# Kernel optimization log

Hardware: AMD Instinct MI355X
Metric: run time of the kernel (lower is better)

Reference implementation:

```python
import jax, jax.numpy as jnp
import numpy as np

B, N, M = 8, 1024, 64          # graphs, ops/graph, machines/graph
OPF, MF = 16, 8                # raw feature dims
H, D, L = 8, 64, 3             # heads, head dim, HGT layers
F = H * D                      # 512 = hidden_dim * num_heads
KC = 8                         # compatible machines per op
NOP, NM = B * N, B * M
EPS = 1e-5


def _graph_ln(x, w, b):
    # PyG LayerNorm(mode='graph') with batch=None: scalar mean/std over the whole tensor
    x = x - x.mean()
    return x / (x.std() + EPS) * w + b


def _seg_softmax(a, idx, n):
    amax = jax.ops.segment_max(a, idx, num_segments=n)
    amax = jnp.where(jnp.isfinite(amax), amax, 0.0)
    ex = jnp.exp(a - amax[idx])
    s = jax.ops.segment_sum(ex, idx, num_segments=n)
    return ex / (s[idx] + 1e-16)


def _forward(op_x, machine_x, W_emb_op, b_emb_op, W_emb_m, b_emb_m,
             opn_w, opn_b, mn_w, mn_b, Wk, bk, Wq, bq, Wv, bv,
             A_rel, M_rel, p_rel, W_out, b_out, skip, ln_w, ln_b,
             ei_precedes, ei_canproc, ei_compat):
    x_op = _graph_ln(op_x @ W_emb_op + b_emb_op, opn_w, opn_b)
    x_m = _graph_ln(machine_x @ W_emb_m + b_emb_m, mn_w, mn_b)
    s0, d0 = ei_precedes   # op -> op
    s1, d1 = ei_canproc    # machine -> op
    s2, d2 = ei_compat     # op -> machine
    scale = 1.0 / jnp.sqrt(jnp.float32(D))
    for l in range(L):
        k_op = (x_op @ Wk[l, 0] + bk[l, 0]).reshape(NOP, H, D)
        q_op = (x_op @ Wq[l, 0] + bq[l, 0]).reshape(NOP, H, D)
        v_op = (x_op @ Wv[l, 0] + bv[l, 0]).reshape(NOP, H, D)
        k_m = (x_m @ Wk[l, 1] + bk[l, 1]).reshape(NM, H, D)
        q_m = (x_m @ Wq[l, 1] + bq[l, 1]).reshape(NM, H, D)
        v_m = (x_m @ Wv[l, 1] + bv[l, 1]).reshape(NM, H, D)
        # relation-specific per-head transforms (a_rel/m_rel of HGTConv)
        k0 = jnp.einsum('nhd,hde->nhe', k_op, A_rel[l, 0]); v0 = jnp.einsum('nhd,hde->nhe', v_op, M_rel[l, 0])
        k1 = jnp.einsum('nhd,hde->nhe', k_m, A_rel[l, 1]);  v1 = jnp.einsum('nhd,hde->nhe', v_m, M_rel[l, 1])
        k2 = jnp.einsum('nhd,hde->nhe', k_op, A_rel[l, 2]); v2 = jnp.einsum('nhd,hde->nhe', v_op, M_rel[l, 2])
        # attention into op nodes: joint softmax over both incoming edge types
        a0 = (q_op[d0] * k0[s0]).sum(-1) * p_rel[l, 0] * scale   # [E0,H]
        a1 = (q_op[d1] * k1[s1]).sum(-1) * p_rel[l, 1] * scale   # [E1,H]
        a_op = jnp.concatenate([a0, a1]); dd = jnp.concatenate([d0, d1])
        w = _seg_softmax(a_op, dd, NOP)
        msg = jnp.concatenate([v0[s0], v1[s1]]) * w[:, :, None]
        agg_op = jax.ops.segment_sum(msg, dd, num_segments=NOP).reshape(NOP, F)
        # attention into machine nodes
        a2 = (q_m[d2] * k2[s2]).sum(-1) * p_rel[l, 2] * scale
        w2 = _seg_softmax(a2, d2, NM)
        agg_m = jax.ops.segment_sum(v2[s2] * w2[:, :, None], d2, num_segments=NM).reshape(NM, F)
        # output projection + learned skip gate (HGTConv internals)
        o_op = jax.nn.gelu(agg_op, approximate=False) @ W_out[l, 0] + b_out[l, 0]
        o_m = jax.nn.gelu(agg_m, approximate=False) @ W_out[l, 1] + b_out[l, 1]
        g_op = jax.nn.sigmoid(skip[l, 0]); g_m = jax.nn.sigmoid(skip[l, 1])
        o_op = g_op * o_op + (1.0 - g_op) * x_op
        o_m = g_m * o_m + (1.0 - g_m) * x_m
        # wrapper residual + dropout(eval=identity) + graph layer norm
        x_op = _graph_ln(o_op + x_op, ln_w[l], ln_b[l])
        x_m = _graph_ln(o_m + x_m, ln_w[l], ln_b[l])
    fea_j = x_op.reshape(B, N, F)
    fea_m = x_m.reshape(B, M, F)
    return fea_j, fea_m, fea_j.mean(1, keepdims=True), fea_m.mean(1, keepdims=True)


def setup_inputs() -> dict:
    key = jax.random.key(0)
    ks = jax.random.split(key, 12)
    rng = np.random.default_rng(0)
    ids = np.arange(NOP).reshape(B, N)
    src0 = ids[:, :-1].ravel(); dst0 = ids[:, 1:].ravel()
    mach = rng.integers(0, M, size=(B, N, KC)) + (np.arange(B) * M)[:, None, None]
    ops = np.broadcast_to(ids[:, :, None], (B, N, KC))
    ei_precedes = jnp.asarray(np.stack([src0, dst0]), dtype=jnp.int32)
    ei_canproc = jnp.asarray(np.stack([mach.ravel(), ops.ravel()]), dtype=jnp.int32)
    ei_compat = jnp.asarray(np.stack([ops.ravel(), mach.ravel()]), dtype=jnp.int32)
    n = lambda k, sh, s=0.05: jax.random.normal(k, sh, dtype=jnp.float32) * s
    return dict(
        op_x=n(ks[0], (NOP, OPF), 1.0),
        machine_x=n(ks[1], (NM, MF), 1.0),
        W_emb_op=n(ks[2], (OPF, F)), b_emb_op=jnp.zeros((F,), jnp.float32),
        W_emb_m=n(ks[3], (MF, F)), b_emb_m=jnp.zeros((F,), jnp.float32),
        opn_w=jnp.ones((F,), jnp.float32), opn_b=jnp.zeros((F,), jnp.float32),
        mn_w=jnp.ones((F,), jnp.float32), mn_b=jnp.zeros((F,), jnp.float32),
        Wk=n(ks[4], (L, 2, F, F)), bk=jnp.zeros((L, 2, F), jnp.float32),
        Wq=n(ks[5], (L, 2, F, F)), bq=jnp.zeros((L, 2, F), jnp.float32),
        Wv=n(ks[6], (L, 2, F, F)), bv=jnp.zeros((L, 2, F), jnp.float32),
        A_rel=n(ks[7], (L, 3, H, D, D)), M_rel=n(ks[8], (L, 3, H, D, D)),
        p_rel=jnp.ones((L, 3, H), jnp.float32),
        W_out=n(ks[9], (L, 2, F, F)), b_out=jnp.zeros((L, 2, F), jnp.float32),
        skip=jnp.ones((L, 2), jnp.float32),
        ln_w=jnp.ones((L, F), jnp.float32), ln_b=jnp.zeros((L, F), jnp.float32),
        ei_precedes=ei_precedes, ei_canproc=ei_canproc, ei_compat=ei_compat,
    )


def reference(op_x, machine_x, W_emb_op, b_emb_op, W_emb_m, b_emb_m,
              opn_w, opn_b, mn_w, mn_b, Wk, bk, Wq, bq, Wv, bv,
              A_rel, M_rel, p_rel, W_out, b_out, skip, ln_w, ln_b,
              ei_precedes, ei_canproc, ei_compat):
    return _forward(op_x, machine_x, W_emb_op, b_emb_op, W_emb_m, b_emb_m,
                    opn_w, opn_b, mn_w, mn_b, Wk, bk, Wq, bq, Wv, bv,
                    A_rel, M_rel, p_rel, W_out, b_out, skip, ln_w, ln_b,
                    ei_precedes, ei_canproc, ei_compat)
```

## Files before the change

### kernel.cpp

```cpp
#include <hip/hip_runtime.h>

typedef unsigned short u16;
typedef __attribute__((ext_vector_type(4))) float floatx4;
typedef __attribute__((ext_vector_type(8))) short shortx8;
typedef __attribute__((ext_vector_type(4))) short shortx4;

#define NOPS 8192
#define NMS  512
#define CQ   2560
#define CM   1536
#define NE2  65536
#define TOPC (NOPS*512)
#define TMC  (NMS*512)

__device__ __forceinline__ float bf2f(u16 u){ return __uint_as_float(((unsigned)u)<<16); }
__device__ __forceinline__ u16 f2bf(float f){
  unsigned u = __float_as_uint(f);
  u += 0x7FFFu + ((u>>16)&1u);
  return (u16)(u>>16);
}
__device__ __forceinline__ float wred(float v){
  #pragma unroll
  for (int o=32;o;o>>=1) v += __shfl_xor(v,o,64);
  return v;
}
__device__ __forceinline__ float wredmax(float v){
  #pragma unroll
  for (int o=32;o;o>>=1) v = fmaxf(v, __shfl_xor(v,o,64));
  return v;
}
__device__ __forceinline__ float geluf(float x){
  return 0.5f*x*(1.f+erff(x*0.70710678118654752f));
}
__device__ __forceinline__ void block_stat_out2(float s, float s2, float* pstat, int slot){
  __shared__ float sb[8];
  s = wred(s); s2 = wred(s2);
  int wv = threadIdx.x >> 6;
  if ((threadIdx.x & 63) == 0){ sb[wv*2] = s; sb[wv*2+1] = s2; }
  __syncthreads();
  if (threadIdx.x == 0){
    float a = 0.f, b = 0.f;
    int nw = blockDim.x >> 6;
    for (int i=0;i<nw;++i){ a += sb[i*2]; b += sb[i*2+1]; }
    pstat[slot*2]   = a;
    pstat[slot*2+1] = b;
  }
}

__global__ __launch_bounds__(256) void cnt2_k(const int* __restrict__ s1, float* __restrict__ Ct,
                                              float* __restrict__ Cn){
  int idx = blockIdx.x*256 + threadIdx.x;
  int n = idx >> 6, l = idx & 63;
  const int* row = s1 + n*8;
  int cnt = 0;
  #pragma unroll
  for (int j=0;j<8;++j) cnt += ((row[j] & 63) == l);
  float f = (float)cnt;
  Cn[(size_t)n*64 + l] = f;
  int b = n >> 10, nl = n & 1023;
  Ct[(size_t)((b<<6) + l)*1024 + nl] = f;
}

__global__ __launch_bounds__(256) void tw_k(const float* __restrict__ Wout, const float* __restrict__ Wq,
                                            u16* __restrict__ Wout_t, u16* __restrict__ Wc_op_t,
                                            u16* __restrict__ Wc_m_t){
  __shared__ u16 t[64][65];
  int g = blockIdx.x;
  const float* s; u16* d;
  if (g < 6){
    s = Wout + (size_t)g*262144;
    d = Wout_t + (size_t)g*262144;
  } else {
    int blk = g - 6; int l = blk >> 1, side = blk & 1;
    s = Wq + (size_t)blk*262144;
    d = side ? (Wc_m_t + (size_t)l*CM*512) : (Wc_op_t + (size_t)l*CQ*512);
  }
  int kb = blockIdx.y*64, nb = blockIdx.z*64;
  int tx = threadIdx.x & 63, ty4 = threadIdx.x >> 6;
  #pragma unroll 4
  for (int p=0;p<16;++p){
    int k = ty4 + p*4;
// ... 78 lines not shown
      int ccl = wn*64 + nt*16 + mrow;
      #pragma unroll
      for (int r2=0;r2<4;++r2){
        int e = wm*32 + mt*16 + quad*4 + r2;
        Wt[(size_t)(rbase + e)*512 + cc0 + ccl] = f2bf(acc[mt][nt][r2]);
      }
    }
  }
}
__global__ void cbias_k(const float* __restrict__ bk, const float* __restrict__ bv,
                        const float* __restrict__ Ar, const float* __restrict__ Mr,
                        float* bias_op, float* bias_m){
  int gx = blockIdx.x; int e = threadIdx.x;
  int l = gx/48; int rem = gx - l*48; int s = rem >> 3; int h = rem & 7;
  int side = (s < 4) ? 0 : 1;
  int r = (s < 4) ? (s+1) : (s-3);
  int useK = side==0 ? (s==0 || s==2) : (s==4);
  int rel  = side==0 ? ((s<2)?0:2) : 1;
  const float* bb  = (useK ? bk : bv) + (size_t)(l*2+side)*512 + h*64;
  const float* Rel = (useK ? Ar : Mr) + ((size_t)(l*3+rel)*8 + h)*4096;
  float acc = 0.f;
  for (int d=0; d<64; ++d) acc += bb[d]*Rel[d*64 + e];
  float* bias = side ? (bias_m + l*CM) : (bias_op + l*CQ);
  bias[r*512 + h*64 + e] = acc;
}

__global__ __launch_bounds__(256) void embed2_k(const float* __restrict__ Xop, const float* __restrict__ Wop,
                                                const float* __restrict__ bop, float* __restrict__ Yop,
                                                const float* __restrict__ Xm, const float* __restrict__ Wm,
                                                const float* __restrict__ bm_, float* __restrict__ Ym,
                                                float* pstat, float* pstat_m){
  int bid = blockIdx.x;
  const float *X, *W, *bias; float *Y, *ps; int K, total, nb, lb;
  if (bid < 1024){ X=Xop; W=Wop; bias=bop; Y=Yop; ps=pstat;   K=16; total=TOPC; nb=1024; lb=bid; }
  else           { X=Xm;  W=Wm;  bias=bm_; Y=Ym;  ps=pstat_m; K=8;  total=TMC;  nb=128;  lb=bid-1024; }
  float s = 0.f, s2 = 0.f;
  for (int idx = lb*256 + threadIdx.x; idx < total; idx += nb*256){
    int n = idx >> 9, f = idx & 511;
    float v = bias[f];
    for (int c=0;c<K;++c) v += X[n*K+c] * W[c*512+f];
    Y[idx] = v;
    s += v; s2 += v*v;
  }
  block_stat_out2(s, s2, ps, lb);
}

__global__ __launch_bounds__(256) void ln2_k(const float* __restrict__ src_op, float* __restrict__ dst_op,
                                             u16* __restrict__ dbf_op, const float* __restrict__ w_op,
                                             const float* __restrict__ b_op,
                                             const float* __restrict__ src_m, float* __restrict__ dst_m,
                                             u16* __restrict__ dbf_m, const float* __restrict__ w_m,
                                             const float* __restrict__ b_m,
                                             const float* __restrict__ pstat, const float* __restrict__ pstat_m,
                                             int nbo, int nbm){
  int bid = blockIdx.x;
  const float *src, *w, *b, *ps; float* dst; u16* dbf; int total4, nb, lb, nblk; float inv_n;
  if (bid < 1024){ src=src_op; dst=dst_op; dbf=dbf_op; w=w_op; b=b_op; ps=pstat;
                   total4=TOPC/4; nb=1024; lb=bid; nblk=nbo; inv_n=1.f/TOPC; }
  else           { src=src_m;  dst=dst_m;  dbf=dbf_m;  w=w_m;  b=b_m;  ps=pstat_m;
                   total4=TMC/4;  nb=128;  lb=bid-1024; nblk=nbm; inv_n=1.f/TMC; }
  __shared__ float sb[8];
  __shared__ float mr[2];
  float s = 0.f, s2 = 0.f;
  for (int i = threadIdx.x; i < nblk; i += 256){ s += ps[2*i]; s2 += ps[2*i+1]; }
  s = wred(s); s2 = wred(s2);
  int wv = threadIdx.x >> 6;
  if ((threadIdx.x & 63) == 0){ sb[wv*2] = s; sb[wv*2+1] = s2; }
  __syncthreads();
  if (threadIdx.x == 0){
    float a = 0.f, bsum = 0.f;
    for (int i=0;i<4;++i){ a += sb[i*2]; bsum += sb[i*2+1]; }
    float mean = a * inv_n;
    float var  = fmaxf(bsum * inv_n - mean*mean, 0.f);
    mr[0] = mean;
    mr[1] = 1.f/(sqrtf(var) + 1e-5f);
  }
  __syncthreads();
  float mean = mr[0], rinv = mr[1];
  const floatx4* s4 = (const floatx4*)src;
  floatx4* d4 = (floatx4*)dst;
  shortx4* db4 = (shortx4*)dbf;
  const floatx4* w4 = (const floatx4*)w;
  const floatx4* b4 = (const floatx4*)b;
  for (int i = lb*256 + threadIdx.x; i < total4; i += nb*256){
    int f = i & 127;
    floatx4 v = s4[i], wv2 = w4[f], bv = b4[f];
    shortx4 sv;
    #pragma unroll
    for (int e=0;e<4;++e){ v[e] = (v[e]-mean)*rinv*wv2[e] + bv[e]; sv[e] = (short)f2bf(v[e]); }
    d4[i] = v;
    db4[i] = sv;
  }
}

__device__ __forceinline__ void gemm_gate_core(u16* As, u16* Bs, const u16* __restrict__ A,
                                               const u16* __restrict__ Bt,
                                               const float* __restrict__ xr, const float* __restrict__ bo,
                                               const float* __restrict__ sk, float* __restrict__ Y,
                                               float* pstat, int slot, int bx, int by){
  const int tid = threadIdx.x;
  const int lane = tid & 63, wave = tid >> 6;
  const int bm = by * 128, bn = bx * 128;
  const int wm = wave & 1, wn = wave >> 1;
  const int mrow = lane & 15, quad = lane >> 4;
  const u16* Ab = A + (size_t)bm*512;
  const u16* Bb = Bt + (size_t)bn*512;
  floatx4 acc[4][4];
  #pragma unroll
  for (int a=0;a<4;++a)
    #pragma unroll
    for (int b=0;b<4;++b) acc[a][b] = (floatx4){0.f,0.f,0.f,0.f};
  const int r0 = tid >> 2, c0 = (tid & 3) * 8;
  const int r1 = (tid+256) >> 2, c1 = ((tid+256) & 3) * 8;
  const int lds0 = wave*512;
  const int lds1 = wave*512 + 2048;
  for (int k0 = 0; k0 < 512; k0 += 32){
    __builtin_amdgcn_global_load_lds((const __attribute__((address_space(1))) void*)(Ab + (size_t)r0*512 + k0 + c0),
                                     (__attribute__((address_space(3))) void*)(As + lds0), 16, 0, 0);
    __builtin_amdgcn_global_load_lds((const __attribute__((address_space(1))) void*)(Ab + (size_t)r1*512 + k0 + c1),
                                     (__attribute__((address_space(3))) void*)(As + lds1), 16, 0, 0);
    __builtin_amdgcn_global_load_lds((const __attribute__((address_space(1))) void*)(Bb + (size_t)r0*512 + k0 + c0),
                                     (__attribute__((address_space(3))) void*)(Bs + lds0), 16, 0, 0);
    __builtin_amdgcn_global_load_lds((const __attribute__((address_space(1))) void*)(Bb + (size_t)r1*512 + k0 + c1),
                                     (__attribute__((address_space(3))) void*)(Bs + lds1), 16, 0, 0);
    __syncthreads();
    shortx8 af[4], bf[4];
    #pragma unroll
    for (int mt=0;mt<4;++mt) af[mt] = *(const shortx8*)(As + (wm*64 + mt*16 + mrow)*32 + quad*8);
    #pragma unroll
    for (int nt=0;nt<4;++nt) bf[nt] = *(const shortx8*)(Bs + (wn*64 + nt*16 + mrow)*32 + quad*8);
    #pragma unroll
    for (int mt=0;mt<4;++mt)
      #pragma unroll
      for (int nt=0;nt<4;++nt)
        acc[mt][nt] = __builtin_amdgcn_mfma_f32_16x16x32_bf16(af[mt], bf[nt], acc[mt][nt], 0, 0, 0);
    __syncthreads();
  }
  float g = 1.f/(1.f+expf(-(*sk)));
  float s = 0.f, s2 = 0.f;
  #pragma unroll
  for (int mt=0;mt<4;++mt){
    #pragma unroll
    for (int nt=0;nt<4;++nt){
      int col = bn + wn*64 + nt*16 + mrow;
// ... 100 lines not shown
    for (int mt=0;mt<4;++mt) af[mt] = *(const shortx8*)(a0 + mt*512);
    #pragma unroll
    for (int nt=0;nt<4;++nt) bf[nt] = *(const shortx8*)(b0 + nt*512);
    stage_half8(Ab, kc1, Obase + 8192, tid);
    MFMA_QUAD(0);
    __builtin_amdgcn_s_barrier();

    #pragma unroll
    for (int mt=0;mt<4;++mt) af[mt] = *(const shortx8*)(a0 + 2048 + mt*512);
    stage_half8(Bb, kc1, Obase + 24576, tid);
    MFMA_QUAD(1);
    asm volatile("s_waitcnt vmcnt(8)" ::: "memory");
    __builtin_amdgcn_s_barrier();

    #pragma unroll
    for (int mt=0;mt<4;++mt) af[mt] = *(const shortx8*)(a0 + 8192 + mt*512);
    #pragma unroll
    for (int nt=0;nt<4;++nt) bf[nt] = *(const shortx8*)(b0 + 8192 + nt*512);
    stage_half8(Ab, kc2, Sbase, tid);
    MFMA_QUAD(0);
    __builtin_amdgcn_s_barrier();

    #pragma unroll
    for (int mt=0;mt<4;++mt) af[mt] = *(const shortx8*)(a0 + 8192 + 2048 + mt*512);
    stage_half8(Bb, kc2, Sbase + 16384, tid);
    MFMA_QUAD(1);
    asm volatile("s_waitcnt vmcnt(8)" ::: "memory");
    __builtin_amdgcn_s_barrier();
  }

  const int crow0 = by*256 + wm*128 + quad*4;
  const int ccol0 = bx*256 + wn*64 + mrow;
  float bv[4];
  #pragma unroll
  for (int nt=0;nt<4;++nt) bv[nt] = bias ? bias[ccol0 + nt*16] : 0.f;
  #pragma unroll
  for (int mh=0;mh<2;++mh){
    #pragma unroll
    for (int mt=0;mt<4;++mt){
      int row = crow0 + mh*64 + mt*16;
      #pragma unroll
      for (int nt=0;nt<4;++nt){
        int col = ccol0 + nt*16;
        #pragma unroll
        for (int r2=0;r2<4;++r2)
          C[(size_t)(row+r2)*N + col] = f2bf(acc[mh*4+mt][nt][r2] + bv[nt]);
      }
    }
  }
}

__global__ __launch_bounds__(256) void qk12_k(const u16* __restrict__ qkv_op, const u16* __restrict__ qkv_m,
                                              const float* __restrict__ prel, const float* __restrict__ Cn,
                                              float* __restrict__ S2f, u16* __restrict__ agg_op){
  __shared__ __align__(16) char smem[37376];
  u16* smem16 = (u16*)smem;
  u16* As = smem16;
  u16* Bs = smem16 + 4608;
  float* Sbuf = (float*)smem;
  u16* P   = smem16 + 9216;
  u16* v1T = smem16 + 13824;
  float* wpreS = (float*)(smem + 36864);
  float* linvS = (float*)(smem + 37120);
  int bh = blockIdx.y; int b = bh >> 3, h = bh & 7;
  int n0 = blockIdx.x * 64;
  int tid = threadIdx.x, lane = tid & 63, wave = tid >> 6;
  int mrow = lane & 15, quad = lane >> 4;
  int wm = wave & 1, wn = wave >> 1;
  int srow = tid >> 2, scol = (tid & 3) * 16;
  if (blockIdx.z == 0){
    float p1 = prel[8 + h] * 0.125f;
    {
      const u16* src = qkv_op + (size_t)(b*1024 + n0 + srow)*CQ + h*64 + scol;
      *(shortx8*)(As + srow*72 + scol)     = *(const shortx8*)(src);
      *(shortx8*)(As + srow*72 + scol + 8) = *(const shortx8*)(src + 8);
    }
    {
      const u16* src = qkv_m + (size_t)(b*64 + srow)*CM + 512 + h*64 + scol;
      *(shortx8*)(Bs + srow*72 + scol)     = *(const shortx8*)(src);
      *(shortx8*)(Bs + srow*72 + scol + 8) = *(const shortx8*)(src + 8);
    }
    {
      const u16* src = qkv_m + (size_t)(b*64 + srow)*CM + 1024 + h*64 + scol;
      shortx8 v0 = *(const shortx8*)(src);
      shortx8 v1 = *(const shortx8*)(src + 8);
      #pragma unroll
      for (int e=0;e<8;++e){ v1T[(scol+e)*72 + srow] = (u16)v0[e]; v1T[(scol+8+e)*72 + srow] = (u16)v1[e]; }
    }
    __syncthreads();
    floatx4 acc[2][2];
    #pragma unroll
    for (int a=0;a<2;++a){ acc[a][0] = (floatx4){0,0,0,0}; acc[a][1] = (floatx4){0,0,0,0}; }
    #pragma unroll
    for (int ks=0; ks<2; ++ks){
      shortx8 af[2], bf[2];
      #pragma unroll
      for (int mt=0;mt<2;++mt) af[mt] = *(const shortx8*)(As + (wm*32 + mt*16 + mrow)*72 + ks*32 + quad*8);
      #pragma unroll
      for (int nt=0;nt<2;++nt) bf[nt] = *(const shortx8*)(Bs + (wn*32 + nt*16 + mrow)*72 + ks*32 + quad*8);
      #pragma unroll
      for (int mt=0;mt<2;++mt)
        #pragma unroll
        for (int nt=0;nt<2;++nt)
          acc[mt][nt] = __builtin_amdgcn_mfma_f32_16x16x32_bf16(af[mt], bf[nt], acc[mt][nt], 0, 0, 0);
    }
    __syncthreads();
    #pragma unroll
    for (int mt=0;mt<2;++mt){
      #pragma unroll
      for (int nt=0;nt<2;++nt){
        int m = wn*32 + nt*16 + mrow;
        #pragma unroll
        for (int r2=0;r2<4;++r2){
          int nl = wm*32 + mt*16 + quad*4 + r2;
          Sbuf[nl*66 + m] = acc[mt][nt][r2] * p1;
        }
      }
    }
    __syncthreads();
    {
      int row = srow;
      int mb  = scol;
      int n_g = b*1024 + n0 + row;
      int nl  = n0 + row;
      float sp = -1e30f;
      if (nl > 0){
        float p0 = prel[h] * 0.125f;
        const u16* qp = qkv_op + (size_t)n_g*CQ + h*64 + mb;
        const u16* kp = qkv_op + (size_t)(n_g-1)*CQ + 512 + h*64 + mb;
        shortx8 qa = *(const shortx8*)(qp), qb2 = *(const shortx8*)(qp + 8);
        shortx8 ka = *(const shortx8*)(kp), kb2 = *(const shortx8*)(kp + 8);
        float d = 0.f;
        #pragma unroll
        for (int e=0;e<8;++e) d += bf2f((u16)qa[e])*bf2f((u16)ka[e]) + bf2f((u16)qb2[e])*bf2f((u16)kb2[e]);
        d += __shfl_xor(d, 1, 64);
        d += __shfl_xor(d, 2, 64);
        sp = d * p0;
      }
      const float* crow = Cn + (size_t)n_g*64 + mb;
      float cv[16];
      float mx = sp;
      #pragma unroll
      for (int j=0;j<16;++j){
        cv[j] = crow[j];
        if (cv[j] > 0.f) mx = fmaxf(mx, Sbuf[row*66 + mb + j]);
      }
      mx = fmaxf(mx, __shfl_xor(mx, 1, 64));
      mx = fmaxf(mx, __shfl_xor(mx, 2, 64));
      float L = 0.f;
      #pragma unroll
      for (int j=0;j<16;j+=4){
        shortx4 pv;
        #pragma unroll
        for (int e=0;e<4;++e){
          float w = (cv[j+e] > 0.f) ? cv[j+e]*expf(Sbuf[row*66 + mb + j + e] - mx) : 0.f;
          L += w;
          pv[e] = (short)f2bf(w);
        }
        *(shortx4*)(P + row*72 + mb + j) = pv;
      }
      L += __shfl_xor(L, 1, 64);
      L += __shfl_xor(L, 2, 64);
      float ep = (nl > 0) ? expf(sp - mx) : 0.f;
      L += ep;
      if ((tid & 3) == 0){ wpreS[row] = ep; linvS[row] = 1.f/(L + 1e-16f); }
    }
    __syncthreads();
    floatx4 po[2][2];
    #pragma unroll
    for (int a=0;a<2;++a){ po[a][0] = (floatx4){0,0,0,0}; po[a][1] = (floatx4){0,0,0,0}; }
    #pragma unroll
    for (int ks=0; ks<2; ++ks){
      shortx8 paf[2], pbf[2];
      #pragma unroll
      for (int mt=0;mt<2;++mt) paf[mt] = *(const shortx8*)(P + (wm*32 + mt*16 + mrow)*72 + ks*32 + quad*8);
      #pragma unroll
      for (int nt=0;nt<2;++nt) pbf[nt] = *(const shortx8*)(v1T + (wn*32 + nt*16 + mrow)*72 + ks*32 + quad*8);
      #pragma unroll
      for (int mt=0;mt<2;++mt)
        #pragma unroll
        for (int nt=0;nt<2;++nt)
          po[mt][nt] = __builtin_amdgcn_mfma_f32_16x16x32_bf16(paf[mt], pbf[nt], po[mt][nt], 0, 0, 0);
    }
    #pragma unroll
    for (int mt=0;mt<2;++mt){
      #pragma unroll
      for (int nt=0;nt<2;++nt){
        int d = wn*32 + nt*16 + mrow;
        #pragma unroll
        for (int r2=0;r2<4;++r2){
          int rl = wm*32 + mt*16 + quad*4 + r2;
          int n = n0 + rl;
          size_t ng = (size_t)b*1024 + n;
          float v = po[mt][nt][r2];
          if (n > 0) v += wpreS[rl] * bf2f(qkv_op[(ng-1)*CQ + 1024 + h*64 + d]);
          v *= linvS[rl];
          agg_op[ng*512 + h*64 + d] = f2bf(geluf(v));
        }
      }
    }
  } else {
    float p2 = prel[16 + h] * 0.125f;
    {
      const u16* src = qkv_m + (size_t)(b*64 + srow)*CM + h*64 + scol;
      *(shortx8*)(As + srow*72 + scol)     = *(const shortx8*)(src);
      *(shortx8*)(As + srow*72 + scol + 8) = *(const shortx8*)(src + 8);
    }
    {
      const u16* src = qkv_op + (size_t)(b*1024 + n0 + srow)*CQ + 1536 + h*64 + scol;
      *(shortx8*)(Bs + srow*72 + scol)     = *(const shortx8*)(src);
      *(shortx8*)(Bs + srow*72 + scol + 8) = *(const shortx8*)(src + 8);
    }
    __syncthreads();
    floatx4 acc[2][2];
    #pragma unroll
    for (int a=0;a<2;++a){ acc[a][0] = (floatx4){0,0,0,0}; acc[a][1] = (floatx4){0,0,0,0}; }
    #pragma unroll
    for (int ks=0; ks<2; ++ks){
      shortx8 af[2], bf[2];
      #pragma unroll
      for (int mt=0;mt<2;++mt) af[mt] = *(const shortx8*)(As + (wm*32 + mt*16 + mrow)*72 + ks*32 + quad*8);
      #pragma unroll
      for (int nt=0;nt<2;++nt) bf[nt] = *(const shortx8*)(Bs + (wn*32 + nt*16 + mrow)*72 + ks*32 + quad*8);
      #pragma unroll
      for (int mt=0;mt<2;++mt)
        #pragma unroll
        for (int nt=0;nt<2;++nt)
          acc[mt][nt] = __builtin_amdgcn_mfma_f32_16x16x32_bf16(af[mt], bf[nt], acc[mt][nt], 0, 0, 0);
    }
    #pragma unroll
    for (int mt=0;mt<2;++mt){
      #pragma unroll
      for (int nt=0;nt<2;++nt){
        int n = wn*32 + nt*16 + mrow;
        #pragma unroll
        for (int r2=0;r2<4;++r2){
          int m = wm*32 + mt*16 + quad*4 + r2;
          S2f[((size_t)(b*64 + m)*8 + h)*1024 + n0 + n] = acc[mt][nt][r2] * p2;
        }
      }
    }
  }
}

__global__ __launch_bounds__(512) void msoftm_k(const float* __restrict__ S2f, const float* __restrict__ Ct,
                                                u16* __restrict__ W2){
  int m = blockIdx.x;
  int h = threadIdx.x >> 6, d = threadIdx.x & 63;
  const float* srow = S2f + ((size_t)m*8 + h)*1024;
  const float* crow = Ct + (size_t)m*1024;
  float s[16], c[16];
  #pragma unroll
  for (int it=0; it<16; ++it){ s[it] = srow[it*64 + d]; c[it] = crow[it*64 + d]; }
  float mx = -1e30f;
  #pragma unroll
  for (int it=0; it<16; ++it) if (c[it] > 0.f) mx = fmaxf(mx, s[it]);
  mx = wredmax(mx);
  float e[16], L = 0.f;
  #pragma unroll
  for (int it=0; it<16; ++it){
    e[it] = (c[it] > 0.f) ? c[it]*expf(s[it]-mx) : 0.f;
    L += e[it];
  }
  L = wred(L);
  float inv = 1.f/(L + 1e-16f);
  u16* wrow = W2 + ((size_t)m*8 + h)*1024;
  #pragma unroll
  for (int it=0; it<16; ++it) wrow[it*64 + d] = f2bf(e[it]*inv);
}

__global__ __launch_bounds__(256) void aggm_k(const u16* __restrict__ qkv_op, const u16* __restrict__ W2,
                                              u16* __restrict__ agg_m){
  __shared__ u16 As[64*40];
  __shared__ u16 Bs[64*40];
  int bh = blockIdx.x; int b = bh >> 3, h = bh & 7;
  int tid = threadIdx.x, lane = tid & 63, wave = tid >> 6;
  int wm = wave & 1, wn = wave >> 1;
  int mrow = lane & 15, quad = lane >> 4;
  floatx4 acc[2][2];
  acc[0][0]=(floatx4){0,0,0,0}; acc[0][1]=(floatx4){0,0,0,0};
  acc[1][0]=(floatx4){0,0,0,0}; acc[1][1]=(floatx4){0,0,0,0};
  const int arow = tid >> 2, acol = (tid & 3) * 8;
  const int nrow = tid >> 3, dcol = (tid & 7) * 8;
  for (int ks = 0; ks < 32; ++ks){
    int nn0 = ks*32;
    *(shortx8*)(As + arow*40 + acol) =
        *(const shortx8*)(W2 + ((size_t)(b*64 + arow)*8 + h)*1024 + nn0 + acol);
    shortx8 vv = *(const shortx8*)(qkv_op + (size_t)(b*1024 + nn0 + nrow)*CQ + 2048 + h*64 + dcol);
    #pragma unroll
    for (int e=0;e<8;++e) Bs[(dcol+e)*40 + nrow] = (u16)vv[e];
    __syncthreads();
    shortx8 af[2], bf[2];
    #pragma unroll
    for (int mt=0;mt<2;++mt) af[mt] = *(const shortx8*)(As + (wm*32 + mt*16 + mrow)*40 + quad*8);
    #pragma unroll
    for (int nt=0;nt<2;++nt) bf[nt] = *(const shortx8*)(Bs + (wn*32 + nt*16 + mrow)*40 + quad*8);
    #pragma unroll
    for (int mt=0;mt<2;++mt)
      #pragma unroll
      for (int nt=0;nt<2;++nt)
        acc[mt][nt] = __builtin_amdgcn_mfma_f32_16x16x32_bf16(af[mt], bf[nt], acc[mt][nt], 0, 0, 0);
    __syncthreads();
  }
  #pragma unroll
  for (int mt=0;mt<2;++mt){
    #pragma unroll
    for (int nt=0;nt<2;++nt){
      int dd = wn*32 + nt*16 + mrow;
      #pragma unroll
      for (int r2=0;r2<4;++r2){
        int m = wm*32 + mt*16 + quad*4 + r2;
        agg_m[(size_t)(b*64 + m)*512 + h*64 + dd] = f2bf(geluf(acc[mt][nt][r2]));
      }
    }
  }
}

__global__ __launch_bounds__(512) void meanj_part_k(const float* __restrict__ xo, float* scratchJ){
  int b = blockIdx.x, chunk = blockIdx.y, f = threadIdx.x;
  float s = 0.f;
  for (int r=0;r<128;++r){
    int row = b*1024 + chunk*128 + r;
    s += xo[(size_t)row*512 + f];
  }
  scratchJ[(b*8 + chunk)*512 + f] = s;
}
__global__ __launch_bounds__(512) void mean2_k(const float* __restrict__ scratchJ, float* __restrict__ out){
  int i = blockIdx.x*512 + threadIdx.x;
  if (i < 4096){
    int b = i >> 9, f = i & 511;
    float s = 0.f;
    #pragma unroll
    for (int c=0;c<8;++c) s += scratchJ[(b*8+c)*512 + f];
    out[4456448 + i] = s * (1.f/1024.f);
  } else {
    int j = i - 4096;
    int b = j >> 9, f = j & 511;
    float s = 0.f;
    for (int r=0;r<64;++r) s += out[(size_t)TOPC + (size_t)(b*64+r)*512 + f];
    out[4460544 + j] = s * (1.f/64.f);
  }
}

extern "C" void kernel_launch(void* const* d_in, const int* in_sizes, int n_in,
                              void* d_out, int out_size, void* d_ws, size_t ws_size,
                              hipStream_t stream){
  const float* op_x      = (const float*)d_in[0];
  const float* machine_x = (const float*)d_in[1];
  const float* W_emb_op  = (const float*)d_in[2];
  const float* b_emb_op  = (const float*)d_in[3];
  const float* W_emb_m   = (const float*)d_in[4];
  const float* b_emb_m   = (const float*)d_in[5];
  const float* opn_w     = (const float*)d_in[6];
  const float* opn_b     = (const float*)d_in[7];
  const float* mn_w      = (const float*)d_in[8];
  const float* mn_b      = (const float*)d_in[9];
  const float* Wk        = (const float*)d_in[10];
  const float* bk        = (const float*)d_in[11];
  const float* Wq        = (const float*)d_in[12];
  const float* bq        = (const float*)d_in[13];
  const float* Wv        = (const float*)d_in[14];
  const float* bv        = (const float*)d_in[15];
  const float* A_rel     = (const float*)d_in[16];
  const float* M_rel     = (const float*)d_in[17];
  const float* p_rel     = (const float*)d_in[18];
  const float* W_out     = (const float*)d_in[19];
  const float* b_out     = (const float*)d_in[20];
  const float* skip      = (const float*)d_in[21];
  const float* ln_w      = (const float*)d_in[22];
  const float* ln_b      = (const float*)d_in[23];
  const int* s1          = (const int*)d_in[25];
  float* out = (float*)d_out;

  char* ws = (char*)d_ws;
  size_t off = 0;
  auto alloc = [&](size_t bytes)->void*{
    void* p = ws + off;
    off = (off + bytes + 255) & ~(size_t)255;
    return p;
  };
  float* pstat     = (float*)alloc(4096*4);
  float* scratchJ  = (float*)alloc(32768*4);
  float* Ct        = (float*)alloc((size_t)NMS*1024*4);
  float* Cn        = (float*)alloc((size_t)NOPS*64*4);
  float* S2f       = (float*)alloc((size_t)NMS*8*1024*4);
  u16*   W2        = (u16*)  alloc((size_t)NMS*8*1024*2);
  float* x_op      = (float*)alloc((size_t)NOPS*512*4);
  u16*   x_op_bf   = (u16*)  alloc((size_t)NOPS*512*2);
  float* x_m       = (float*)alloc((size_t)NMS*512*4);
  u16*   x_m_bf    = (u16*)  alloc((size_t)NMS*512*2);
  u16*   qkv_op    = (u16*)  alloc((size_t)NOPS*CQ*2);
  u16*   qkv_m     = (u16*)  alloc((size_t)NMS*CM*2);
  u16*   agg_op    = (u16*)  alloc((size_t)NOPS*512*2);
  u16*   agg_m     = (u16*)  alloc((size_t)NMS*512*2);
  u16*   Wc_op_t   = (u16*)  alloc((size_t)3*CQ*512*2);
  float* bias_op   = (float*)alloc((size_t)3*CQ*4);
  u16*   Wc_m_t    = (u16*)  alloc((size_t)3*CM*512*2);
  float* bias_m    = (float*)alloc((size_t)3*CM*4);
  u16*   Wout_t    = (u16*)  alloc((size_t)6*262144*2);
  float* o_op      = (float*)qkv_op;
  float* o_m       = (float*)qkv_m;
  float* pstat_m   = pstat + 2048;

  cnt2_k<<<2048,256,0,stream>>>(s1, Ct, Cn);
  tw_k<<<dim3(12,8,8),256,0,stream>>>(W_out, Wq, Wout_t, Wc_op_t, Wc_m_t);
  qb_k<<<12,256,0,stream>>>(bq, bias_op, bias_m);
  combine3_k<<<dim3(144,4),256,0,stream>>>(Wk, Wv, A_rel, M_rel, Wc_op_t, Wc_m_t);
  cbias_k<<<144,64,0,stream>>>(bk, bv, A_rel, M_rel, bias_op, bias_m);

  embed2_k<<<1152,256,0,stream>>>(op_x, W_emb_op, b_emb_op, x_op,
                                  machine_x, W_emb_m, b_emb_m, x_m, pstat, pstat_m);
  ln2_k<<<1152,256,0,stream>>>(x_op, x_op, x_op_bf, opn_w, opn_b,
                               x_m, x_m, x_m_bf, mn_w, mn_b, pstat, pstat_m, 1024, 128);

  for (int l=0; l<3; ++l){
    int last = (l == 2);
    gemm8_k<<<332,512,131072,stream>>>(x_op_bf, Wc_op_t + (size_t)l*CQ*512, bias_op + l*CQ, qkv_op, CQ, 10, 320,
                                       x_m_bf, Wc_m_t + (size_t)l*CM*512, bias_m + l*CM, qkv_m, CM, 6);
    qk12_k<<<dim3(16,64,2),256,0,stream>>>(qkv_op, qkv_m, p_rel + l*24, Cn, S2f, agg_op);
    msoftm_k<<<NMS,512,0,stream>>>(S2f, Ct, W2);
    aggm_k<<<64,256,0,stream>>>(qkv_op, W2, agg_m);
    gemmgate2_k<<<272,256,0,stream>>>(agg_op, Wout_t + (size_t)(l*2+0)*262144, x_op,
                                      b_out + (size_t)(l*2+0)*512, skip + l*2+0, o_op, pstat, 256,
                                      agg_m, Wout_t + (size_t)(l*2+1)*262144, x_m,
                                      b_out + (size_t)(l*2+1)*512, skip + l*2+1, o_m, pstat_m);
    ln2_k<<<1152,256,0,stream>>>(o_op, last ? out : x_op, x_op_bf, ln_w + l*512, ln_b + l*512,
                                 o_m, last ? (out + TOPC) : x_m, x_m_bf, ln_w + l*512, ln_b + l*512,
                                 pstat, pstat_m, 256, 16);
  }

  meanj_part_k<<<dim3(8,8),512,0,stream>>>(out, scratchJ);
  mean2_k<<<16,512,0,stream>>>(scratchJ, out);
}
```

Baseline: 589.1 us.

## Fuse machine-side attention into one flash-style kernel and skip final bf16 store

The machine-side attention path used to run as three steps: qk12_k's z=1 branch wrote fp32 scores to S2f, msoftm_k computed a masked softmax into W2, and aggm_k did the weighted V aggregation. A new mattn_k replaces all three. Each block takes 16 machines for one head, makes two passes over the op keys (first the max, then exp-weighted accumulation of P·V with MFMA), and applies GELU at the end. This removes the S2f/W2 global round trips and two kernel launches, at the cost of recomputing QK scores in the second pass and running only 256 blocks. Separately, ln2_k no longer writes the bf16 copy after the last layer, since nothing reads it.

```diff
diff --git a/kernel.cpp b/kernel.cpp
--- a/kernel.cpp
+++ b/kernel.cpp
@@ -9,7 +9,6 @@
 #define NMS  512
 #define CQ   2560
 #define CM   1536
-#define NE2  65536
 #define TOPC (NOPS*512)
 #define TMC  (NMS*512)
 
@@ -22,11 +21,6 @@
 __device__ __forceinline__ float wred(float v){
   #pragma unroll
   for (int o=32;o;o>>=1) v += __shfl_xor(v,o,64);
-  return v;
-}
-__device__ __forceinline__ float wredmax(float v){
-  #pragma unroll
-  for (int o=32;o;o>>=1) v = fmaxf(v, __shfl_xor(v,o,64));
   return v;
 }
 __device__ __forceinline__ float geluf(float x){
@@ -211,7 +205,7 @@
                                              u16* __restrict__ dbf_m, const float* __restrict__ w_m,
                                              const float* __restrict__ b_m,
                                              const float* __restrict__ pstat, const float* __restrict__ pstat_m,
-                                             int nbo, int nbm){
+                                             int nbo, int nbm, int wbf){
   int bid = blockIdx.x;
   const float *src, *w, *b, *ps; float* dst; u16* dbf; int total4, nb, lb, nblk; float inv_n;
   if (bid < 1024){ src=src_op; dst=dst_op; dbf=dbf_op; w=w_op; b=b_op; ps=pstat;
@@ -248,7 +242,7 @@
     #pragma unroll
     for (int e=0;e<4;++e){ v[e] = (v[e]-mean)*rinv*wv2[e] + bv[e]; sv[e] = (short)f2bf(v[e]); }
     d4[i] = v;
-    db4[i] = sv;
+    if (wbf) db4[i] = sv;
   }
 }
 
@@ -455,7 +449,7 @@
 
 __global__ __launch_bounds__(256) void qk12_k(const u16* __restrict__ qkv_op, const u16* __restrict__ qkv_m,
                                               const float* __restrict__ prel, const float* __restrict__ Cn,
-                                              float* __restrict__ S2f, u16* __restrict__ agg_op){
+                                              u16* __restrict__ agg_op){
   __shared__ __align__(16) char smem[37376];
   u16* smem16 = (u16*)smem;
   u16* As = smem16;
@@ -471,251 +465,242 @@
   int mrow = lane & 15, quad = lane >> 4;
   int wm = wave & 1, wn = wave >> 1;
   int srow = tid >> 2, scol = (tid & 3) * 16;
-  if (blockIdx.z == 0){
-    float p1 = prel[8 + h] * 0.125f;
-    {
-      const u16* src = qkv_op + (size_t)(b*1024 + n0 + srow)*CQ + h*64 + scol;
-      *(shortx8*)(As + srow*72 + scol)     = *(const shortx8*)(src);
-      *(shortx8*)(As + srow*72 + scol + 8) = *(const shortx8*)(src + 8);
-    }
-    {
-      const u16* src = qkv_m + (size_t)(b*64 + srow)*CM + 512 + h*64 + scol;
-      *(shortx8*)(Bs + srow*72 + scol)     = *(const shortx8*)(src);
-      *(shortx8*)(Bs + srow*72 + scol + 8) = *(const shortx8*)(src + 8);
-    }
-    {
-      const u16* src = qkv_m + (size_t)(b*64 + srow)*CM + 1024 + h*64 + scol;
-      shortx8 v0 = *(const shortx8*)(src);
-      shortx8 v1 = *(const shortx8*)(src + 8);
-      #pragma unroll
-      for (int e=0;e<8;++e){ v1T[(scol+e)*72 + srow] = (u16)v0[e]; v1T[(scol+8+e)*72 + srow] = (u16)v1[e]; }
-    }
-    __syncthreads();
-    floatx4 acc[2][2];
-    #pragma unroll
-    for (int a=0;a<2;++a){ acc[a][0] = (floatx4){0,0,0,0}; acc[a][1] = (floatx4){0,0,0,0}; }
-    #pragma unroll
-    for (int ks=0; ks<2; ++ks){
-      shortx8 af[2], bf[2];
-      #pragma unroll
-      for (int mt=0;mt<2;++mt) af[mt] = *(const shortx8*)(As + (wm*32 + mt*16 + mrow)*72 + ks*32 + quad*8);
-      #pragma unroll
-      for (int nt=0;nt<2;++nt) bf[nt] = *(const shortx8*)(Bs + (wn*32 + nt*16 + mrow)*72 + ks*32 + quad*8);
-      #pragma unroll
-      for (int mt=0;mt<2;++mt)
-        #pragma unroll
-        for (int nt=0;nt<2;++nt)
-          acc[mt][nt] = __builtin_amdgcn_mfma_f32_16x16x32_bf16(af[mt], bf[nt], acc[mt][nt], 0, 0, 0);
-    }
-    __syncthreads();
-    #pragma unroll
-    for (int mt=0;mt<2;++mt){
-      #pragma unroll
-      for (int nt=0;nt<2;++nt){
-        int m = wn*32 + nt*16 + mrow;
-        #pragma unroll
-        for (int r2=0;r2<4;++r2){
-          int nl = wm*32 + mt*16 + quad*4 + r2;
-          Sbuf[nl*66 + m] = acc[mt][nt][r2] * p1;
-        }
-      }
-    }
-    __syncthreads();
-    {
-      int row = srow;
-      int mb  = scol;
-      int n_g = b*1024 + n0 + row;
-      int nl  = n0 + row;
-      float sp = -1e30f;
-      if (nl > 0){
-        float p0 = prel[h] * 0.125f;
-        const u16* qp = qkv_op + (size_t)n_g*CQ + h*64 + mb;
-        const u16* kp = qkv_op + (size_t)(n_g-1)*CQ + 512 + h*64 + mb;
-        shortx8 qa = *(const shortx8*)(qp), qb2 = *(const shortx8*)(qp + 8);
-        shortx8 ka = *(const shortx8*)(kp), kb2 = *(const shortx8*)(kp + 8);
-        float d = 0.f;
-        #pragma unroll
-        for (int e=0;e<8;++e) d += bf2f((u16)qa[e])*bf2f((u16)ka[e]) + bf2f((u16)qb2[e])*bf2f((u16)kb2[e]);
-        d += __shfl_xor(d, 1, 64);
-        d += __shfl_xor(d, 2, 64);
-        sp = d * p0;
-      }
-      const float* crow = Cn + (size_t)n_g*64 + mb;
-      float cv[16];
-      float mx = sp;
-      #pragma unroll
-      for (int j=0;j<16;++j){
-        cv[j] = crow[j];
-        if (cv[j] > 0.f) mx = fmaxf(mx, Sbuf[row*66 + mb + j]);
-      }
-      mx = fmaxf(mx, __shfl_xor(mx, 1, 64));
-      mx = fmaxf(mx, __shfl_xor(mx, 2, 64));
-      float L = 0.f;
-      #pragma unroll
-      for (int j=0;j<16;j+=4){
-        shortx4 pv;
-        #pragma unroll
-        for (int e=0;e<4;++e){
-          float w = (cv[j+e] > 0.f) ? cv[j+e]*expf(Sbuf[row*66 + mb + j + e] - mx) : 0.f;
-          L += w;
-          pv[e] = (short)f2bf(w);
-        }
-        *(shortx4*)(P + row*72 + mb + j) = pv;
-      }
-      L += __shfl_xor(L, 1, 64);
-      L += __shfl_xor(L, 2, 64);
-      float ep = (nl > 0) ? expf(sp - mx) : 0.f;
-      L += ep;
-      if ((tid & 3) == 0){ wpreS[row] = ep; linvS[row] = 1.f/(L + 1e-16f); }
-    }
-    __syncthreads();
-    floatx4 po[2][2];
-    #pragma unroll
-    for (int a=0;a<2;++a){ po[a][0] = (floatx4){0,0,0,0}; po[a][1] = (floatx4){0,0,0,0}; }
-    #pragma unroll
-    for (int ks=0; ks<2; ++ks){
-      shortx8 paf[2], pbf[2];
-      #pragma unroll
-      for (int mt=0;mt<2;++mt) paf[mt] = *(const shortx8*)(P + (wm*32 + mt*16 + mrow)*72 + ks*32 + quad*8);
-      #pragma unroll
-      for (int nt=0;nt<2;++nt) pbf[nt] = *(const shortx8*)(v1T + (wn*32 + nt*16 + mrow)*72 + ks*32 + quad*8);
-      #pragma unroll
-      for (int mt=0;mt<2;++mt)
-        #pragma unroll
-        for (int nt=0;nt<2;++nt)
-          po[mt][nt] = __builtin_amdgcn_mfma_f32_16x16x32_bf16(paf[mt], pbf[nt], po[mt][nt], 0, 0, 0);
-    }
-    #pragma unroll
-    for (int mt=0;mt<2;++mt){
-      #pragma unroll
-      for (int nt=0;nt<2;++nt){
-        int d = wn*32 + nt*16 + mrow;
-        #pragma unroll
-        for (int r2=0;r2<4;++r2){
-          int rl = wm*32 + mt*16 + quad*4 + r2;
-          int n = n0 + rl;
-          size_t ng = (size_t)b*1024 + n;
-          float v = po[mt][nt][r2];
-          if (n > 0) v += wpreS[rl] * bf2f(qkv_op[(ng-1)*CQ + 1024 + h*64 + d]);
-          v *= linvS[rl];
-          agg_op[ng*512 + h*64 + d] = f2bf(geluf(v));
-        }
-      }
-    }
-  } else {
-    float p2 = prel[16 + h] * 0.125f;
-    {
-      const u16* src = qkv_m + (size_t)(b*64 + srow)*CM + h*64 + scol;
-      *(shortx8*)(As + srow*72 + scol)     = *(const shortx8*)(src);
-      *(shortx8*)(As + srow*72 + scol + 8) = *(const shortx8*)(src + 8);
-    }
-    {
-      const u16* src = qkv_op + (size_t)(b*1024 + n0 + srow)*CQ + 1536 + h*64 + scol;
-      *(shortx8*)(Bs + srow*72 + scol)     = *(const shortx8*)(src);
-      *(shortx8*)(Bs + srow*72 + scol + 8) = *(const shortx8*)(src + 8);
-    }
-    __syncthreads();
-    floatx4 acc[2][2];
-    #pragma unroll
-    for (int a=0;a<2;++a){ acc[a][0] = (floatx4){0,0,0,0}; acc[a][1] = (floatx4){0,0,0,0}; }
-    #pragma unroll
-    for (int ks=0; ks<2; ++ks){
-      shortx8 af[2], bf[2];
-      #pragma unroll
-      for (int mt=0;mt<2;++mt) af[mt] = *(const shortx8*)(As + (wm*32 + mt*16 + mrow)*72 + ks*32 + quad*8);
-      #pragma unroll
-      for (int nt=0;nt<2;++nt) bf[nt] = *(const shortx8*)(Bs + (wn*32 + nt*16 + mrow)*72 + ks*32 + quad*8);
-      #pragma unroll
-      for (int mt=0;mt<2;++mt)
-        #pragma unroll
-        for (int nt=0;nt<2;++nt)
-          acc[mt][nt] = __builtin_amdgcn_mfma_f32_16x16x32_bf16(af[mt], bf[nt], acc[mt][nt], 0, 0, 0);
-    }
-    #pragma unroll
-    for (int mt=0;mt<2;++mt){
-      #pragma unroll
-      for (int nt=0;nt<2;++nt){
-        int n = wn*32 + nt*16 + mrow;
-        #pragma unroll
-        for (int r2=0;r2<4;++r2){
-          int m = wm*32 + mt*16 + quad*4 + r2;
-          S2f[((size_t)(b*64 + m)*8 + h)*1024 + n0 + n] = acc[mt][nt][r2] * p2;
-        }
-      }
-    }
-  }
-}
-
-__global__ __launch_bounds__(512) void msoftm_k(const float* __restrict__ S2f, const float* __restrict__ Ct,
-                                                u16* __restrict__ W2){
-  int m = blockIdx.x;
-  int h = threadIdx.x >> 6, d = threadIdx.x & 63;
-  const float* srow = S2f + ((size_t)m*8 + h)*1024;
-  const float* crow = Ct + (size_t)m*1024;
-  float s[16], c[16];
-  #pragma unroll
-  for (int it=0; it<16; ++it){ s[it] = srow[it*64 + d]; c[it] = crow[it*64 + d]; }
-  float mx = -1e30f;
-  #pragma unroll
-  for (int it=0; it<16; ++it) if (c[it] > 0.f) mx = fmaxf(mx, s[it]);
-  mx = wredmax(mx);
-  float e[16], L = 0.f;
-  #pragma unroll
-  for (int it=0; it<16; ++it){
-    e[it] = (c[it] > 0.f) ? c[it]*expf(s[it]-mx) : 0.f;
-    L += e[it];
-  }
-  L = wred(L);
-  float inv = 1.f/(L + 1e-16f);
-  u16* wrow = W2 + ((size_t)m*8 + h)*1024;
-  #pragma unroll
-  for (int it=0; it<16; ++it) wrow[it*64 + d] = f2bf(e[it]*inv);
-}
-
-__global__ __launch_bounds__(256) void aggm_k(const u16* __restrict__ qkv_op, const u16* __restrict__ W2,
-                                              u16* __restrict__ agg_m){
-  __shared__ u16 As[64*40];
-  __shared__ u16 Bs[64*40];
-  int bh = blockIdx.x; int b = bh >> 3, h = bh & 7;
-  int tid = threadIdx.x, lane = tid & 63, wave = tid >> 6;
-  int wm = wave & 1, wn = wave >> 1;
-  int mrow = lane & 15, quad = lane >> 4;
+  float p1 = prel[8 + h] * 0.125f;
+  {
+    const u16* src = qkv_op + (size_t)(b*1024 + n0 + srow)*CQ + h*64 + scol;
+    *(shortx8*)(As + srow*72 + scol)     = *(const shortx8*)(src);
+    *(shortx8*)(As + srow*72 + scol + 8) = *(const shortx8*)(src + 8);
+  }
+  {
+    const u16* src = qkv_m + (size_t)(b*64 + srow)*CM + 512 + h*64 + scol;
+    *(shortx8*)(Bs + srow*72 + scol)     = *(const shortx8*)(src);
+    *(shortx8*)(Bs + srow*72 + scol + 8) = *(const shortx8*)(src + 8);
+  }
+  {
+    const u16* src = qkv_m + (size_t)(b*64 + srow)*CM + 1024 + h*64 + scol;
+    shortx8 v0 = *(const shortx8*)(src);
+    shortx8 v1 = *(const shortx8*)(src + 8);
+    #pragma unroll
+    for (int e=0;e<8;++e){ v1T[(scol+e)*72 + srow] = (u16)v0[e]; v1T[(scol+8+e)*72 + srow] = (u16)v1[e]; }
+  }
+  __syncthreads();
   floatx4 acc[2][2];
-  acc[0][0]=(floatx4){0,0,0,0}; acc[0][1]=(floatx4){0,0,0,0};
-  acc[1][0]=(floatx4){0,0,0,0}; acc[1][1]=(floatx4){0,0,0,0};
-  const int arow = tid >> 2, acol = (tid & 3) * 8;
-  const int nrow = tid >> 3, dcol = (tid & 7) * 8;
-  for (int ks = 0; ks < 32; ++ks){
-    int nn0 = ks*32;
-    *(shortx8*)(As + arow*40 + acol) =
-        *(const shortx8*)(W2 + ((size_t)(b*64 + arow)*8 + h)*1024 + nn0 + acol);
-    shortx8 vv = *(const shortx8*)(qkv_op + (size_t)(b*1024 + nn0 + nrow)*CQ + 2048 + h*64 + dcol);
-    #pragma unroll
-    for (int e=0;e<8;++e) Bs[(dcol+e)*40 + nrow] = (u16)vv[e];
-    __syncthreads();
+  #pragma unroll
+  for (int a=0;a<2;++a){ acc[a][0] = (floatx4){0,0,0,0}; acc[a][1] = (floatx4){0,0,0,0}; }
+  #pragma unroll
+  for (int ks=0; ks<2; ++ks){
     shortx8 af[2], bf[2];
     #pragma unroll
-    for (int mt=0;mt<2;++mt) af[mt] = *(const shortx8*)(As + (wm*32 + mt*16 + mrow)*40 + quad*8);
-    #pragma unroll
-    for (int nt=0;nt<2;++nt) bf[nt] = *(const shortx8*)(Bs + (wn*32 + nt*16 + mrow)*40 + quad*8);
+    for (int mt=0;mt<2;++mt) af[mt] = *(const shortx8*)(As + (wm*32 + mt*16 + mrow)*72 + ks*32 + quad*8);
+    #pragma unroll
+    for (int nt=0;nt<2;++nt) bf[nt] = *(const shortx8*)(Bs + (wn*32 + nt*16 + mrow)*72 + ks*32 + quad*8);
     #pragma unroll
     for (int mt=0;mt<2;++mt)
       #pragma unroll
       for (int nt=0;nt<2;++nt)
         acc[mt][nt] = __builtin_amdgcn_mfma_f32_16x16x32_bf16(af[mt], bf[nt], acc[mt][nt], 0, 0, 0);
+  }
+  __syncthreads();
+  #pragma unroll
+  for (int mt=0;mt<2;++mt){
+    #pragma unroll
+    for (int nt=0;nt<2;++nt){
+      int m = wn*32 + nt*16 + mrow;
+      #pragma unroll
+      for (int r2=0;r2<4;++r2){
+        int nl = wm*32 + mt*16 + quad*4 + r2;
+        Sbuf[nl*66 + m] = acc[mt][nt][r2] * p1;
+      }
+    }
+  }
+  __syncthreads();
+  {
+    int row = srow;
+    int mb  = scol;
+    int n_g = b*1024 + n0 + row;
+    int nl  = n0 + row;
+    float sp = -1e30f;
+    if (nl > 0){
+      float p0 = prel[h] * 0.125f;
+      const u16* qp = qkv_op + (size_t)n_g*CQ + h*64 + mb;
+      const u16* kp = qkv_op + (size_t)(n_g-1)*CQ + 512 + h*64 + mb;
+      shortx8 qa = *(const shortx8*)(qp), qb2 = *(const shortx8*)(qp + 8);
+      shortx8 ka = *(const shortx8*)(kp), kb2 = *(const shortx8*)(kp + 8);
+      float d = 0.f;
+      #pragma unroll
+      for (int e=0;e<8;++e) d += bf2f((u16)qa[e])*bf2f((u16)ka[e]) + bf2f((u16)qb2[e])*bf2f((u16)kb2[e]);
+      d += __shfl_xor(d, 1, 64);
+      d += __shfl_xor(d, 2, 64);
+      sp = d * p0;
+    }
+    const float* crow = Cn + (size_t)n_g*64 + mb;
+    float cv[16];
+    float mx = sp;
+    #pragma unroll
+    for (int j=0;j<16;++j){
+      cv[j] = crow[j];
+      if (cv[j] > 0.f) mx = fmaxf(mx, Sbuf[row*66 + mb + j]);
+    }
+    mx = fmaxf(mx, __shfl_xor(mx, 1, 64));
+    mx = fmaxf(mx, __shfl_xor(mx, 2, 64));
+    float L = 0.f;
+    #pragma unroll
+    for (int j=0;j<16;j+=4){
+      shortx4 pv;
+      #pragma unroll
+      for (int e=0;e<4;++e){
+        float w = (cv[j+e] > 0.f) ? cv[j+e]*expf(Sbuf[row*66 + mb + j + e] - mx) : 0.f;
+        L += w;
+        pv[e] = (short)f2bf(w);
+      }
+      *(shortx4*)(P + row*72 + mb + j) = pv;
+    }
+    L += __shfl_xor(L, 1, 64);
+    L += __shfl_xor(L, 2, 64);
+    float ep = (nl > 0) ? expf(sp - mx) : 0.f;
+    L += ep;
+    if ((tid & 3) == 0){ wpreS[row] = ep; linvS[row] = 1.f/(L + 1e-16f); }
+  }
+  __syncthreads();
+  floatx4 po[2][2];
+  #pragma unroll
+  for (int a=0;a<2;++a){ po[a][0] = (floatx4){0,0,0,0}; po[a][1] = (floatx4){0,0,0,0}; }
+  #pragma unroll
+  for (int ks=0; ks<2; ++ks){
+    shortx8 paf[2], pbf[2];
+    #pragma unroll
+    for (int mt=0;mt<2;++mt) paf[mt] = *(const shortx8*)(P + (wm*32 + mt*16 + mrow)*72 + ks*32 + quad*8);
+    #pragma unroll
+    for (int nt=0;nt<2;++nt) pbf[nt] = *(const shortx8*)(v1T + (wn*32 + nt*16 + mrow)*72 + ks*32 + quad*8);
+    #pragma unroll
+    for (int mt=0;mt<2;++mt)
+      #pragma unroll
+      for (int nt=0;nt<2;++nt)
+        po[mt][nt] = __builtin_amdgcn_mfma_f32_16x16x32_bf16(paf[mt], pbf[nt], po[mt][nt], 0, 0, 0);
+  }
+  #pragma unroll
+  for (int mt=0;mt<2;++mt){
+    #pragma unroll
+    for (int nt=0;nt<2;++nt){
+      int d = wn*32 + nt*16 + mrow;
+      #pragma unroll
+      for (int r2=0;r2<4;++r2){
+        int rl = wm*32 + mt*16 + quad*4 + r2;
+        int n = n0 + rl;
+        size_t ng = (size_t)b*1024 + n;
+        float v = po[mt][nt][r2];
+        if (n > 0) v += wpreS[rl] * bf2f(qkv_op[(ng-1)*CQ + 1024 + h*64 + d]);
+        v *= linvS[rl];
+        agg_op[ng*512 + h*64 + d] = f2bf(geluf(v));
+      }
+    }
+  }
+}
+
+__global__ __launch_bounds__(256) void mattn_k(const u16* __restrict__ qkv_op, const u16* __restrict__ qkv_m,
+                                               const float* __restrict__ prel, const float* __restrict__ Ct,
+                                               u16* __restrict__ agg_m){
+  __shared__ __align__(16) u16 qs[16*72];
+  __shared__ __align__(16) u16 ks[128*72];
+  __shared__ __align__(16) u16 vsT[64*136];
+  __shared__ __align__(16) u16 Ps[16*136];
+  __shared__ float redv[2][4][16];
+  int g = blockIdx.x; int bh = blockIdx.y; int b = bh >> 3, h = bh & 7;
+  int tid = threadIdx.x, lane = tid & 63, w = tid >> 6;
+  int mrow = lane & 15, quad = lane >> 4;
+  float p2 = prel[16 + h] * 0.125f;
+  if (tid < 128){
+    int r = tid >> 3, cg = (tid & 7) * 8;
+    *(shortx8*)(qs + r*72 + cg) = *(const shortx8*)(qkv_m + (size_t)(b*64 + g*16 + r)*CM + h*64 + cg);
+  }
+  const float* ctbase = Ct + (size_t)(b*64 + g*16 + mrow)*1024;
+  float mx = -1e30f;
+  for (int ch = 0; ch < 8; ++ch){
+    int nb = ch*128;
+    #pragma unroll
+    for (int i=0;i<4;++i){
+      int idx = i*256 + tid;
+      int r = idx >> 3, cg = (idx & 7) * 8;
+      *(shortx8*)(ks + r*72 + cg) =
+        *(const shortx8*)(qkv_op + (size_t)(b*1024 + nb + r)*CQ + 1536 + h*64 + cg);
+    }
     __syncthreads();
-  }
-  #pragma unroll
-  for (int mt=0;mt<2;++mt){
-    #pragma unroll
-    for (int nt=0;nt<2;++nt){
-      int dd = wn*32 + nt*16 + mrow;
+    #pragma unroll
+    for (int nt=0; nt<2; ++nt){
+      floatx4 acc = (floatx4){0,0,0,0};
+      #pragma unroll
+      for (int kk=0; kk<2; ++kk){
+        shortx8 af = *(const shortx8*)(ks + (w*32 + nt*16 + mrow)*72 + kk*32 + quad*8);
+        shortx8 bf = *(const shortx8*)(qs + mrow*72 + kk*32 + quad*8);
+        acc = __builtin_amdgcn_mfma_f32_16x16x32_bf16(af, bf, acc, 0, 0, 0);
+      }
+      int nloc = w*32 + nt*16 + quad*4;
+      floatx4 cv = *(const floatx4*)(ctbase + nb + nloc);
+      #pragma unroll
+      for (int r2=0;r2<4;++r2)
+        if (cv[r2] > 0.f) mx = fmaxf(mx, acc[r2]*p2);
+    }
+    __syncthreads();
+  }
+  mx = fmaxf(mx, __shfl_xor(mx, 16, 64));
+  mx = fmaxf(mx, __shfl_xor(mx, 32, 64));
+  if (lane < 16) redv[0][w][lane] = mx;
+  __syncthreads();
+  mx = fmaxf(fmaxf(redv[0][0][mrow], redv[0][1][mrow]), fmaxf(redv[0][2][mrow], redv[0][3][mrow]));
+  float L = 0.f;
+  floatx4 O = (floatx4){0,0,0,0};
+  for (int ch = 0; ch < 8; ++ch){
+    int nb = ch*128;
+    #pragma unroll
+    for (int i=0;i<4;++i){
+      int idx = i*256 + tid;
+      int r = idx >> 3, cg = (idx & 7) * 8;
+      *(shortx8*)(ks + r*72 + cg) =
+        *(const shortx8*)(qkv_op + (size_t)(b*1024 + nb + r)*CQ + 1536 + h*64 + cg);
+      shortx8 vv = *(const shortx8*)(qkv_op + (size_t)(b*1024 + nb + r)*CQ + 2048 + h*64 + cg);
+      #pragma unroll
+      for (int e=0;e<8;++e) vsT[(cg+e)*136 + r] = (u16)vv[e];
+    }
+    __syncthreads();
+    #pragma unroll
+    for (int nt=0; nt<2; ++nt){
+      floatx4 acc = (floatx4){0,0,0,0};
+      #pragma unroll
+      for (int kk=0; kk<2; ++kk){
+        shortx8 af = *(const shortx8*)(ks + (w*32 + nt*16 + mrow)*72 + kk*32 + quad*8);
+        shortx8 bf = *(const shortx8*)(qs + mrow*72 + kk*32 + quad*8);
+        acc = __builtin_amdgcn_mfma_f32_16x16x32_bf16(af, bf, acc, 0, 0, 0);
+      }
+      int nloc = w*32 + nt*16 + quad*4;
+      floatx4 cv = *(const floatx4*)(ctbase + nb + nloc);
+      shortx4 pv;
       #pragma unroll
       for (int r2=0;r2<4;++r2){
-        int m = wm*32 + mt*16 + quad*4 + r2;
-        agg_m[(size_t)(b*64 + m)*512 + h*64 + dd] = f2bf(geluf(acc[mt][nt][r2]));
+        float e = (cv[r2] > 0.f) ? cv[r2]*expf(acc[r2]*p2 - mx) : 0.f;
+        L += e;
+        pv[r2] = (short)f2bf(e);
       }
-    }
+      *(shortx4*)(Ps + mrow*136 + nloc) = pv;
+    }
+    __syncthreads();
+    #pragma unroll
+    for (int kk=0; kk<4; ++kk){
+      shortx8 af = *(const shortx8*)(Ps + mrow*136 + kk*32 + quad*8);
+      shortx8 bf = *(const shortx8*)(vsT + (w*16 + mrow)*136 + kk*32 + quad*8);
+      O = __builtin_amdgcn_mfma_f32_16x16x32_bf16(af, bf, O, 0, 0, 0);
+    }
+    __syncthreads();
+  }
+  L += __shfl_xor(L, 16, 64);
+  L += __shfl_xor(L, 32, 64);
+  if (lane < 16) redv[1][w][lane] = L;
+  __syncthreads();
+  #pragma unroll
+  for (int r2=0;r2<4;++r2){
+    int m = quad*4 + r2;
+    float Ls = redv[1][0][m] + redv[1][1][m] + redv[1][2][m] + redv[1][3][m];
+    float v = O[r2] / (Ls + 1e-16f);
+    agg_m[(size_t)(b*64 + g*16 + m)*512 + h*64 + w*16 + mrow] = f2bf(geluf(v));
   }
 }
 
@@ -786,8 +771,6 @@
   float* scratchJ  = (float*)alloc(32768*4);
   float* Ct        = (float*)alloc((size_t)NMS*1024*4);
   float* Cn        = (float*)alloc((size_t)NOPS*64*4);
-  float* S2f       = (float*)alloc((size_t)NMS*8*1024*4);
-  u16*   W2        = (u16*)  alloc((size_t)NMS*8*1024*2);
   float* x_op      = (float*)alloc((size_t)NOPS*512*4);
   u16*   x_op_bf   = (u16*)  alloc((size_t)NOPS*512*2);
   float* x_m       = (float*)alloc((size_t)NMS*512*4);
@@ -814,22 +797,21 @@
   embed2_k<<<1152,256,0,stream>>>(op_x, W_emb_op, b_emb_op, x_op,
                                   machine_x, W_emb_m, b_emb_m, x_m, pstat, pstat_m);
   ln2_k<<<1152,256,0,stream>>>(x_op, x_op, x_op_bf, opn_w, opn_b,
-                               x_m, x_m, x_m_bf, mn_w, mn_b, pstat, pstat_m, 1024, 128);
+                               x_m, x_m, x_m_bf, mn_w, mn_b, pstat, pstat_m, 1024, 128, 1);
 
   for (int l=0; l<3; ++l){
     int last = (l == 2);
     gemm8_k<<<332,512,131072,stream>>>(x_op_bf, Wc_op_t + (size_t)l*CQ*512, bias_op + l*CQ, qkv_op, CQ, 10, 320,
                                        x_m_bf, Wc_m_t + (size_t)l*CM*512, bias_m + l*CM, qkv_m, CM, 6);
-    qk12_k<<<dim3(16,64,2),256,0,stream>>>(qkv_op, qkv_m, p_rel + l*24, Cn, S2f, agg_op);
-    msoftm_k<<<NMS,512,0,stream>>>(S2f, Ct, W2);
-    aggm_k<<<64,256,0,stream>>>(qkv_op, W2, agg_m);
+    qk12_k<<<dim3(16,64),256,0,stream>>>(qkv_op, qkv_m, p_rel + l*24, Cn, agg_op);
+    mattn_k<<<dim3(4,64),256,0,stream>>>(qkv_op, qkv_m, p_rel + l*24, Ct, agg_m);
     gemmgate2_k<<<272,256,0,stream>>>(agg_op, Wout_t + (size_t)(l*2+0)*262144, x_op,
                                       b_out + (size_t)(l*2+0)*512, skip + l*2+0, o_op, pstat, 256,
                                       agg_m, Wout_t + (size_t)(l*2+1)*262144, x_m,
                                       b_out + (size_t)(l*2+1)*512, skip + l*2+1, o_m, pstat_m);
     ln2_k<<<1152,256,0,stream>>>(o_op, last ? out : x_op, x_op_bf, ln_w + l*512, ln_b + l*512,
                                  o_m, last ? (out + TOPC) : x_m, x_m_bf, ln_w + l*512, ln_b + l*512,
-                                 pstat, pstat_m, 256, 16);
+                                 pstat, pstat_m, 256, 16, last ? 0 : 1);
   }
 
   meanj_part_k<<<dim3(8,8),512,0,stream>>>(out, scratchJ);
```

Result: faster. 574.2 us (-2.5%).
